# Kernel tuning notes

Measured on AMD Instinct MI355X. Metric: run time of the kernel, lower is better.

The kernel has to match this reference:

```python
import jax, jax.numpy as jnp
import numpy as np

N = 8192
D = 512
N_SLICE = 64
K = 8
H = 30 * K  # 240


def _gen_k_slice(rng):
    xx = rng.normal(0.0, 1.0, (N_SLICE, K, D))
    slices = np.zeros((N_SLICE, K, D), dtype=np.float64)
    for i in range(N_SLICE):
        _, _, vh = np.linalg.svd(xx[i], full_matrices=False)
        slices[i] = vh
    return slices.astype(np.float32)


def setup_inputs() -> dict:
    key = jax.random.key(0)
    k1, k2, k3, k4, k5, k6, k7 = jax.random.split(key, 7)
    rng = np.random.default_rng(0)
    # conv weights: PyTorch Conv1d default init ~ U(-s, s), s = 1/sqrt(fan_in)
    s1 = 1.0 / np.sqrt(K)
    s3 = 1.0 / np.sqrt(H)
    return {
        "X": jax.random.normal(k1, (N, D), dtype=jnp.float32),
        "Y": jax.random.normal(k2, (N, D), dtype=jnp.float32),
        "X_noise": jax.random.normal(k3, (N, N_SLICE * K), dtype=jnp.float32),
        "thetas": jnp.asarray(_gen_k_slice(rng)),                     # [S, K, D]
        "W1": jax.random.uniform(k4, (N_SLICE, H, K), jnp.float32, -s1, s1),
        "b1": jax.random.uniform(k5, (N_SLICE, H), jnp.float32, -s1, s1),
        "W3": jax.random.uniform(k6, (N_SLICE, H), jnp.float32, -s3, s3),
        "b3": jax.random.uniform(k7, (N_SLICE,), jnp.float32, -s3, s3),
        "sigma_noise": 0,
    }


def _mlp(sample, W1, b1, W3, b3):
    # sample: [N, S, K] -> grouped 1x1 conv k->H, relu, grouped conv H->1
    h1 = jax.nn.relu(jnp.einsum('nsk,shk->nsh', sample, W1) + b1[None])
    return jnp.einsum('nsh,sh->ns', h1, W3) + b3[None]  # [N, S]


def reference(X, Y, X_noise, thetas, W1, b1, W3, b3, sigma_noise):
    # batched per-slice projections (fuses the n_slice matmul loop)
    x_sample = jnp.einsum('nd,skd->nsk', X, thetas)  # [N, S, K]
    y_sample = jnp.einsum('nd,skd->nsk', Y, thetas)
    if sigma_noise > 0:
        x_sample = x_sample + sigma_noise * X_noise.reshape(X.shape[0], N_SLICE, K)
    pred_x = _mlp(x_sample, W1, b1, W3, b3)  # [N, S]
    pred_y = _mlp(y_sample, W1, b1, W3, b3)
    n_y = pred_y.shape[0]
    ret = jnp.mean(pred_x, axis=0) - jax.nn.logsumexp(
        pred_y - jnp.log(jnp.float32(n_y)), axis=0)
    return jnp.mean(-ret)
```

## Files before the change

kernel.cpp:

```cpp
#include <hip/hip_runtime.h>
#include <hip/hip_bf16.h>

#define NROWS 8192
#define DDIM  512
#define NS    64
#define KK    8
#define HH    240
#define SP2   72
#define STG   4096

typedef __attribute__((ext_vector_type(8))) _Float16 f16x8;
typedef __attribute__((ext_vector_type(4))) _Float16 f16x4;
typedef __attribute__((ext_vector_type(4))) float f32x4;
typedef __attribute__((ext_vector_type(2))) float f32x2;

typedef __attribute__((address_space(3))) void       lds_void;
typedef const __attribute__((address_space(1))) void gbl_cvoid;

__device__ inline unsigned pk2u(float a, float b) {
    auto h = __builtin_amdgcn_cvt_pkrtz(a, b);
    unsigned u;
    __builtin_memcpy(&u, &h, sizeof(u));
    return u;
}

__device__ inline void gl16(const ushort* g, ushort* l) {
    __builtin_amdgcn_global_load_lds((gbl_cvoid*)g, (lds_void*)l, 16, 0, 0);
}

#define XN (NROWS * DDIM)
__global__ __launch_bounds__(256)
void pack_kernel(const float* __restrict__ X, const float* __restrict__ Y,
                 const float* __restrict__ Th, const float* __restrict__ W1,
                 ushort* __restrict__ Xh, ushort* __restrict__ Yh,
                 ushort* __restrict__ Thh, ushort* __restrict__ W1h)
{
    int i = (blockIdx.x * 256 + threadIdx.x) * 4;
    const float* src; ushort* dst; int off;
    if (i < XN)               { src = X;  dst = Xh;  off = i; }
    else if (i < 2 * XN)      { src = Y;  dst = Yh;  off = i - XN; }
    else if (i < 2 * XN + 262144) { src = Th; dst = Thh; off = i - 2 * XN; }
    else                      { src = W1; dst = W1h; off = i - (2 * XN + 262144); }
    float4 v = *(const float4*)(src + off);
    *(uint2*)(dst + off) = make_uint2(pk2u(v.x, v.y), pk2u(v.z, v.w));
}

__global__ __launch_bounds__(256, 4)
void proj_mlp_kernel(const ushort* __restrict__ Xh,
                     const ushort* __restrict__ Yh,
                     const float* __restrict__ Xn,
                     const ushort* __restrict__ Thh,
                     const ushort* __restrict__ W1h,
                     const float* __restrict__ b1,
                     const float* __restrict__ W3,
                     const float* __restrict__ sig_p,
                     float* __restrict__ sumx,
                     float* __restrict__ maxy,
                     float* __restrict__ sey)
{
    __shared__ __align__(16) ushort smem[3 * STG];
    ushort* sl = smem;

    const int tid  = threadIdx.x;
    const int w    = __builtin_amdgcn_readfirstlane(tid >> 6);
    const int lane = tid & 63;
    const int bx   = blockIdx.x;
    const int by   = blockIdx.y;

    const bool isX = (bx < 128);
    const int  bxl = isX ? bx : (bx - 128);
    const ushort* srcA = (isX ? Xh : Yh) + (size_t)bxl * 64 * DDIM;

    const int grow = (w << 4) + (lane >> 2);
    const int gchk = (lane & 3) ^ ((grow >> 1) & 3);
    const ushort* gA = srcA + (size_t)grow * DDIM + gchk * 8;
    const ushort* gB = Thh + (size_t)(by * 64 + grow) * DDIM + gchk * 8;
    const int woff = w * 512;

    f32x4 acc[2][2];
#pragma unroll
    for (int m = 0; m < 2; ++m)
#pragma unroll
        for (int n = 0; n < 2; ++n) acc[m][n] = (f32x4){0.f, 0.f, 0.f, 0.f};

    const int wr  = (w >> 1) * 32;
    const int wc  = (w & 1) * 32;
    const int r16 = lane & 15;
    const int hi4 = lane >> 4;

    int offA[2], offB[2];
#pragma unroll
    for (int m = 0; m < 2; ++m) {
        int row = wr + m * 16 + r16;
        offA[m] = row * 32 + ((hi4 ^ ((row >> 1) & 3)) * 8);
    }
#pragma unroll
    for (int n = 0; n < 2; ++n) {
        int row = wc + n * 16 + r16;
        offB[n] = 2048 + row * 32 + ((hi4 ^ ((row >> 1) & 3)) * 8);
    }

    gl16(gA,      &smem[woff]);
    gl16(gB,      &smem[2048 + woff]);
    gl16(gA + 32, &smem[STG + woff]);
    gl16(gB + 32, &smem[STG + 2048 + woff]);

#pragma unroll
    for (int kt = 0; kt < 16; ++kt) {
        if (kt < 15)
            asm volatile("s_waitcnt vmcnt(2)\n\ts_barrier" ::: "memory");
        else
            asm volatile("s_waitcnt vmcnt(0)\n\ts_barrier" ::: "memory");

        if (kt < 14) {
            const int st = ((kt + 2) % 3) * STG;
            gl16(gA + (kt + 2) * 32, &smem[st + woff]);
            gl16(gB + (kt + 2) * 32, &smem[st + 2048 + woff]);
        }

        const int cur = (kt % 3) * STG;
        f16x8 af[2], bfv[2];
#pragma unroll
        for (int m = 0; m < 2; ++m) af[m]  = *(const f16x8*)(smem + cur + offA[m]);
#pragma unroll
        for (int n = 0; n < 2; ++n) bfv[n] = *(const f16x8*)(smem + cur + offB[n]);
#pragma unroll
        for (int m = 0; m < 2; ++m)
#pragma unroll
            for (int n = 0; n < 2; ++n)
                acc[m][n] = __builtin_amdgcn_mfma_f32_16x16x32_f16(
                    af[m], bfv[n], acc[m][n], 0, 0, 0);
    }
    __syncthreads();

    const float sig = *sig_p;
    const bool addnoise = (sig > 0.f) && isX;
    const int n0g = bxl * 64;

#pragma unroll
    for (int m = 0; m < 2; ++m)
#pragma unroll
        for (int n = 0; n < 2; ++n) {
            const int col  = wc + n * 16 + r16;
            const int rowb = wr + m * 16 + hi4 * 4;
            float v[4];
#pragma unroll
            for (int j = 0; j < 4; ++j) {
                v[j] = acc[m][n][j];
                if (addnoise)
                    v[j] = fmaf(sig, Xn[(size_t)(n0g + rowb + j) * (NS * KK) + by * 64 + col], v[j]);
            }
            unsigned u01 = pk2u(v[0], v[1]);
            unsigned u23 = pk2u(v[2], v[3]);
            sl[(rowb + 0) * SP2 + col] = (ushort)u01;
            sl[(rowb + 1) * SP2 + col] = (ushort)(u01 >> 16);
            sl[(rowb + 2) * SP2 + col] = (ushort)u23;
            sl[(rowb + 3) * SP2 + col] = (ushort)(u23 >> 16);
        }
    __syncthreads();

#pragma unroll 1
    for (int si = 0; si < 2; ++si) {
        const int sloc = w * 2 + si;
        const int s    = by * 8 + sloc;

        f16x4 bsamp[4];
#pragma unroll
        for (int nt = 0; nt < 4; ++nt) {
            f16x4 t = {0, 0, 0, 0};
            if (hi4 < 2)
                t = *(const f16x4*)(sl + (nt * 16 + r16) * SP2 + sloc * 8 + hi4 * 4);
            bsamp[nt] = t;
        }

        const ushort* w1p = W1h + (size_t)s * HH * KK;
        const float*  b1p = b1 + s * HH;
        const float*  w3p = W3 + s * HH;

        f32x2 pn2[4];
#pragma unroll
        for (int nt = 0; nt < 4; ++nt) pn2[nt] = (f32x2){0.f, 0.f};

#pragma unroll 5
        for (int ht = 0; ht < HH / 16; ++ht) {
            f16x4 aw = {0, 0, 0, 0};
            if (hi4 < 2)
                aw = *(const f16x4*)(w1p + (ht * 16 + r16) * 8 + hi4 * 4);
            float4 b4 = *(const float4*)(b1p + ht * 16 + hi4 * 4);
            float4 w4 = *(const float4*)(w3p + ht * 16 + hi4 * 4);
            f32x4 z   = (f32x4){b4.x, b4.y, b4.z, b4.w};
            f32x2 w01 = (f32x2){w4.x, w4.y};
            f32x2 w23 = (f32x2){w4.z, w4.w};
            const f32x2 zero2 = (f32x2){0.f, 0.f};
#pragma unroll
            for (int nt = 0; nt < 4; ++nt) {
                f32x4 t = __builtin_amdgcn_mfma_f32_16x16x16f16(aw, bsamp[nt], z, 0, 0, 0);
                f32x2 t01 = (f32x2){t[0], t[1]};
                f32x2 t23 = (f32x2){t[2], t[3]};
                t01 = __builtin_elementwise_max(t01, zero2);
                t23 = __builtin_elementwise_max(t23, zero2);
                pn2[nt] = __builtin_elementwise_fma(t01, w01, pn2[nt]);
                pn2[nt] = __builtin_elementwise_fma(t23, w23, pn2[nt]);
            }
        }

        if (isX) {
            float lsum = 0.f;
#pragma unroll
            for (int nt = 0; nt < 4; ++nt) lsum += pn2[nt].x + pn2[nt].y;
#pragma unroll
            for (int off = 1; off < 64; off <<= 1)
                lsum += __shfl_xor(lsum, off);
            if (lane == 0) sumx[s * 128 + bxl] = lsum;
        } else {
            float p[4];
#pragma unroll
            for (int nt = 0; nt < 4; ++nt) {
                f32x2 v = pn2[nt];
                v.x += __shfl_xor(v.x, 16);
                v.y += __shfl_xor(v.y, 16);
                v.x += __shfl_xor(v.x, 32);
                v.y += __shfl_xor(v.y, 32);
                p[nt] = v.x + v.y;
            }
            float M = fmaxf(fmaxf(p[0], p[1]), fmaxf(p[2], p[3]));
            float se = __expf(p[0] - M) + __expf(p[1] - M)
                     + __expf(p[2] - M) + __expf(p[3] - M);
#pragma unroll
            for (int off = 1; off < 16; off <<= 1) {
                float Mo = __shfl_xor(M, off);
                float so = __shfl_xor(se, off);
                float Mm = fmaxf(M, Mo);
                se = se * __expf(M - Mm) + so * __expf(Mo - Mm);
                M = Mm;
            }
            if (lane == 0) {
                maxy[s * 128 + bxl] = M;
                sey[s * 128 + bxl]  = se;
            }
        }
    }
}

__global__ __launch_bounds__(256)
void final_kernel(const float* __restrict__ sumx,
                  const float* __restrict__ maxy,
                  const float* __restrict__ sey,
                  float* __restrict__ out)
{
    __shared__ float term_s[NS];
    const int tid = threadIdx.x;
    const int s = tid >> 2, q = tid & 3;
    const int base = s * 128 + q * 32;

    float sum = 0.f, M = -3.4e38f;
#pragma unroll 8
    for (int i = 0; i < 32; ++i) {
        sum += sumx[base + i];
        M = fmaxf(M, maxy[base + i]);
    }
    float se = 0.f;
#pragma unroll 8
    for (int i = 0; i < 32; ++i)
        se += sey[base + i] * __expf(maxy[base + i] - M);

#pragma unroll
    for (int off = 1; off < 4; off <<= 1) {
        float Mo = __shfl_xor(M, off);
        float so = __shfl_xor(se, off);
        float su = __shfl_xor(sum, off);
        float Mm = fmaxf(M, Mo);
        se = se * __expf(M - Mm) + so * __expf(Mo - Mm);
        M = Mm;
        sum += su;
    }
    if (q == 0)
        term_s[s] = M + logf(se) - logf((float)NROWS) - sum * (1.0f / (float)NROWS);
    __syncthreads();
    if (tid < 64) {
        float v = term_s[tid];
#pragma unroll
        for (int off = 1; off < 64; off <<= 1) v += __shfl_xor(v, off);
        if (tid == 0) out[0] = v * (1.0f / (float)NS);
    }
}

extern "C" void kernel_launch(void* const* d_in, const int* in_sizes, int n_in,
                              void* d_out, int out_size, void* d_ws, size_t ws_size,
                              hipStream_t stream)
{
    const float* X   = (const float*)d_in[0];
    const float* Y   = (const float*)d_in[1];
    const float* Xn  = (const float*)d_in[2];
    const float* Th  = (const float*)d_in[3];
    const float* W1  = (const float*)d_in[4];
    const float* b1  = (const float*)d_in[5];
    const float* W3  = (const float*)d_in[6];
    const float* sig = (const float*)d_in[8];

    ushort* Xh   = (ushort*)d_ws;
    ushort* Yh   = Xh + XN;
    ushort* Thh  = Yh + XN;
    ushort* W1h  = Thh + 262144;
    float*  sumx = (float*)(W1h + 122880);
    float*  maxy = sumx + NS * 128;
    float*  sey  = maxy + NS * 128;

    pack_kernel<<<(2 * XN + 262144 + 122880) / 1024, 256, 0, stream>>>(
        X, Y, Th, W1, Xh, Yh, Thh, W1h);

    dim3 g1(256, 8, 1);
    proj_mlp_kernel<<<g1, 256, 0, stream>>>(Xh, Yh, Xn, Thh, W1h, b1, W3,
                                            sig, sumx, maxy, sey);
    final_kernel<<<1, 256, 0, stream>>>(sumx, maxy, sey, (float*)d_out);
}
```

Before: 65.27 us.

## Widen projection tile to 128 columns so each block covers 16 slices

Each block now projects its 64 rows against 128 theta rows (16 slices) instead of 64, halving grid.y and so halving how often the X/Y tiles are re-read from global memory. The LDS staging grows to three 6144-element stages, each wave keeps a 2x4 MFMA accumulator tile, and each wave runs the MLP over 4 slices instead of 2. The cost is fewer blocks (1024 instead of 2048), more registers and LDS per block, and a longer serial MLP phase per wave, which could reduce occupancy and latency hiding.

```diff
diff --git a/kernel.cpp b/kernel.cpp
--- a/kernel.cpp
+++ b/kernel.cpp
@@ -6,8 +6,9 @@
 #define NS    64
 #define KK    8
 #define HH    240
-#define SP2   72
-#define STG   4096
+#define SP    136
+#define ARGN  2048
+#define STG   6144
 
 typedef __attribute__((ext_vector_type(8))) _Float16 f16x8;
 typedef __attribute__((ext_vector_type(4))) _Float16 f16x4;
@@ -70,64 +71,65 @@
     const bool isX = (bx < 128);
     const int  bxl = isX ? bx : (bx - 128);
     const ushort* srcA = (isX ? Xh : Yh) + (size_t)bxl * 64 * DDIM;
+    const ushort* srcB = Thh + (size_t)by * 128 * DDIM;
 
     const int grow = (w << 4) + (lane >> 2);
     const int gchk = (lane & 3) ^ ((grow >> 1) & 3);
-    const ushort* gA = srcA + (size_t)grow * DDIM + gchk * 8;
-    const ushort* gB = Thh + (size_t)(by * 64 + grow) * DDIM + gchk * 8;
+    const ushort* gA  = srcA + (size_t)grow * DDIM + gchk * 8;
+    const ushort* gB0 = srcB + (size_t)grow * DDIM + gchk * 8;
+    const ushort* gB1 = srcB + (size_t)(grow + 64) * DDIM + gchk * 8;
     const int woff = w * 512;
 
-    f32x4 acc[2][2];
+#define ISSUE(kf, st) { const int k_ = (kf) * 32; ushort* s_ = smem + (st); \
+    gl16(gA  + k_, s_ + woff); \
+    gl16(gB0 + k_, s_ + ARGN + woff); \
+    gl16(gB1 + k_, s_ + ARGN + 2048 + woff); }
+
+    f32x4 acc[2][4];
 #pragma unroll
     for (int m = 0; m < 2; ++m)
 #pragma unroll
-        for (int n = 0; n < 2; ++n) acc[m][n] = (f32x4){0.f, 0.f, 0.f, 0.f};
+        for (int n = 0; n < 4; ++n) acc[m][n] = (f32x4){0.f, 0.f, 0.f, 0.f};
 
     const int wr  = (w >> 1) * 32;
-    const int wc  = (w & 1) * 32;
+    const int wc  = (w & 1) * 64;
     const int r16 = lane & 15;
     const int hi4 = lane >> 4;
 
-    int offA[2], offB[2];
+    int offA[2], offB[4];
 #pragma unroll
     for (int m = 0; m < 2; ++m) {
         int row = wr + m * 16 + r16;
         offA[m] = row * 32 + ((hi4 ^ ((row >> 1) & 3)) * 8);
     }
 #pragma unroll
-    for (int n = 0; n < 2; ++n) {
+    for (int n = 0; n < 4; ++n) {
         int row = wc + n * 16 + r16;
-        offB[n] = 2048 + row * 32 + ((hi4 ^ ((row >> 1) & 3)) * 8);
-    }
-
-    gl16(gA,      &smem[woff]);
-    gl16(gB,      &smem[2048 + woff]);
-    gl16(gA + 32, &smem[STG + woff]);
-    gl16(gB + 32, &smem[STG + 2048 + woff]);
+        offB[n] = ARGN + row * 32 + ((hi4 ^ ((row >> 1) & 3)) * 8);
+    }
+
+    ISSUE(0, 0);
+    ISSUE(1, STG);
 
 #pragma unroll
     for (int kt = 0; kt < 16; ++kt) {
         if (kt < 15)
-            asm volatile("s_waitcnt vmcnt(2)\n\ts_barrier" ::: "memory");
+            asm volatile("s_waitcnt vmcnt(3)\n\ts_barrier" ::: "memory");
         else
             asm volatile("s_waitcnt vmcnt(0)\n\ts_barrier" ::: "memory");
 
-        if (kt < 14) {
-            const int st = ((kt + 2) % 3) * STG;
-            gl16(gA + (kt + 2) * 32, &smem[st + woff]);
-            gl16(gB + (kt + 2) * 32, &smem[st + 2048 + woff]);
-        }
+        if (kt < 14) ISSUE(kt + 2, ((kt + 2) % 3) * STG);
 
         const int cur = (kt % 3) * STG;
-        f16x8 af[2], bfv[2];
+        f16x8 af[2], bfv[4];
 #pragma unroll
         for (int m = 0; m < 2; ++m) af[m]  = *(const f16x8*)(smem + cur + offA[m]);
 #pragma unroll
-        for (int n = 0; n < 2; ++n) bfv[n] = *(const f16x8*)(smem + cur + offB[n]);
+        for (int n = 0; n < 4; ++n) bfv[n] = *(const f16x8*)(smem + cur + offB[n]);
 #pragma unroll
         for (int m = 0; m < 2; ++m)
 #pragma unroll
-            for (int n = 0; n < 2; ++n)
+            for (int n = 0; n < 4; ++n)
                 acc[m][n] = __builtin_amdgcn_mfma_f32_16x16x32_f16(
                     af[m], bfv[n], acc[m][n], 0, 0, 0);
     }
@@ -140,7 +142,7 @@
 #pragma unroll
     for (int m = 0; m < 2; ++m)
 #pragma unroll
-        for (int n = 0; n < 2; ++n) {
+        for (int n = 0; n < 4; ++n) {
             const int col  = wc + n * 16 + r16;
             const int rowb = wr + m * 16 + hi4 * 4;
             float v[4];
@@ -148,28 +150,28 @@
             for (int j = 0; j < 4; ++j) {
                 v[j] = acc[m][n][j];
                 if (addnoise)
-                    v[j] = fmaf(sig, Xn[(size_t)(n0g + rowb + j) * (NS * KK) + by * 64 + col], v[j]);
+                    v[j] = fmaf(sig, Xn[(size_t)(n0g + rowb + j) * (NS * KK) + by * 128 + col], v[j]);
             }
             unsigned u01 = pk2u(v[0], v[1]);
             unsigned u23 = pk2u(v[2], v[3]);
-            sl[(rowb + 0) * SP2 + col] = (ushort)u01;
-            sl[(rowb + 1) * SP2 + col] = (ushort)(u01 >> 16);
-            sl[(rowb + 2) * SP2 + col] = (ushort)u23;
-            sl[(rowb + 3) * SP2 + col] = (ushort)(u23 >> 16);
+            sl[(rowb + 0) * SP + col] = (ushort)u01;
+            sl[(rowb + 1) * SP + col] = (ushort)(u01 >> 16);
+            sl[(rowb + 2) * SP + col] = (ushort)u23;
+            sl[(rowb + 3) * SP + col] = (ushort)(u23 >> 16);
         }
     __syncthreads();
 
 #pragma unroll 1
-    for (int si = 0; si < 2; ++si) {
-        const int sloc = w * 2 + si;
-        const int s    = by * 8 + sloc;
+    for (int si = 0; si < 4; ++si) {
+        const int sloc = w * 4 + si;
+        const int s    = by * 16 + sloc;
 
         f16x4 bsamp[4];
 #pragma unroll
         for (int nt = 0; nt < 4; ++nt) {
             f16x4 t = {0, 0, 0, 0};
             if (hi4 < 2)
-                t = *(const f16x4*)(sl + (nt * 16 + r16) * SP2 + sloc * 8 + hi4 * 4);
+                t = *(const f16x4*)(sl + (nt * 16 + r16) * SP + sloc * 8 + hi4 * 4);
             bsamp[nt] = t;
         }
 
@@ -309,7 +311,7 @@
     pack_kernel<<<(2 * XN + 262144 + 122880) / 1024, 256, 0, stream>>>(
         X, Y, Th, W1, Xh, Yh, Thh, W1h);
 
-    dim3 g1(256, 8, 1);
+    dim3 g1(256, 4, 1);
     proj_mlp_kernel<<<g1, 256, 0, stream>>>(Xh, Yh, Xn, Thh, W1h, b1, W3,
                                             sig, sumx, maxy, sey);
     final_kernel<<<1, 256, 0, stream>>>(sumx, maxy, sey, (float*)d_out);
```

After: 65.48 us. Within noise of the previous version (+0.3%).
